# Kernel optimization log

Hardware: AMD Instinct MI355X
Metric: run time of the kernel (lower is better)

Reference implementation:

```python
import jax, jax.numpy as jnp
import numpy as np
from jax import lax

C = 256
HEADS = 8
HD = C // HEADS  # 32
D = 32  # max(L=32, C//16)
KERNELS = [1, 3, 5, 7]
EPS = 1e-5


def setup_inputs() -> dict:
    key = jax.random.key(0)
    ks = jax.random.split(key, 16)
    inp = {
        'x': jax.random.normal(ks[0], (8, C, 32, 32), jnp.float32),
        'qkv_w': jax.random.normal(ks[1], (3 * C, C), jnp.float32) * 0.05,
        'out_w': jax.random.normal(ks[2], (C, C), jnp.float32) * 0.05,
        'conv_w1': jax.random.normal(ks[3], (C, C, 1, 1), jnp.float32) * 0.05,
        'conv_w3': jax.random.normal(ks[4], (C, C, 3, 3), jnp.float32) * 0.05,
        'conv_w5': jax.random.normal(ks[5], (C, C, 5, 5), jnp.float32) * 0.05,
        'conv_w7': jax.random.normal(ks[6], (C, C, 7, 7), jnp.float32) * 0.05,
        'conv_b': jax.random.normal(ks[7], (4, C), jnp.float32) * 0.05,
        'bn_gamma': jax.random.uniform(ks[8], (4, C), jnp.float32, 0.5, 1.5),
        'bn_beta': jax.random.normal(ks[9], (4, C), jnp.float32) * 0.05,
        'bn_mean': jax.random.normal(ks[10], (4, C), jnp.float32) * 0.05,
        'bn_var': jax.random.uniform(ks[11], (4, C), jnp.float32, 0.5, 1.5),
        'fc_w': jax.random.normal(ks[12], (D, C), jnp.float32) * 0.05,
        'fc_b': jax.random.normal(ks[13], (D,), jnp.float32) * 0.05,
        'fcs_w': jax.random.normal(ks[14], (4, C, D), jnp.float32) * 0.05,
        'fcs_b': jax.random.normal(ks[15], (4, C), jnp.float32) * 0.05,
    }
    return inp


def _conv_bn_relu(x, w, b, g, beta, m, v):
    k = w.shape[-1]
    y = lax.conv_general_dilated(
        x, w, window_strides=(1, 1), padding=[(k // 2, k // 2)] * 2,
        dimension_numbers=('NCHW', 'OIHW', 'NCHW'))
    y = y + b[None, :, None, None]
    inv = g / jnp.sqrt(v + EPS)  # eval-mode batchnorm
    y = y * inv[None, :, None, None] + (beta - m * inv)[None, :, None, None]
    return jax.nn.relu(y)


def reference(x, qkv_w, out_w, conv_w1, conv_w3, conv_w5, conv_w7, conv_b,
              bn_gamma, bn_beta, bn_mean, bn_var, fc_w, fc_b, fcs_w, fcs_b):
    bsz, ch, ht, wd = x.shape
    n = ht * wd
    xf = x.reshape(bsz, ch, n)
    qkv = jnp.einsum('oc,bcn->bon', qkv_w, xf)  # [b, 3C, N] (1x1 conv)
    q, k, v = jnp.split(qkv, 3, axis=1)
    q = q.reshape(bsz, HEADS, HD, n)
    k = k.reshape(bsz, HEADS, HD, n)
    v = v.reshape(bsz, HEADS, HD, n)
    scale = 1.0 / np.sqrt(HD)
    scores = jnp.einsum('bhdi,bhdj->bhij', q, k) * scale  # [b,h,N,N]
    probs = jax.nn.softmax(scores, axis=-1)
    ctx = jnp.einsum('bhij,bhdj->bhdi', probs, v)  # [b,h,hd,N]
    ctx = ctx.reshape(bsz, ch, ht, wd)
    out = jnp.einsum('oc,bcn->bon', out_w, ctx.reshape(bsz, ch, n)).reshape(bsz, ch, ht, wd)

    ws = [conv_w1, conv_w3, conv_w5, conv_w7]
    feats = jnp.stack([
        _conv_bn_relu(out, ws[i], conv_b[i], bn_gamma[i], bn_beta[i], bn_mean[i], bn_var[i])
        for i in range(4)
    ], axis=0)  # [4, b, C, H, W]
    U = feats.sum(axis=0)
    S = U.mean(axis=(-2, -1))  # [b, C]
    Z = S @ fc_w.T + fc_b  # [b, D]
    logits = jnp.einsum('kcd,bd->kbc', fcs_w, Z) + fcs_b[:, None, :]  # [4,b,C]
    attn = jax.nn.softmax(logits, axis=0)[:, :, :, None, None]  # softmax over kernel branches
    V = (attn * feats).sum(axis=0)  # [b, C, H, W]
    return V
```

## Files before the change

### kernel.cpp

```cpp
#include <hip/hip_runtime.h>
#include <math.h>


typedef __attribute__((ext_vector_type(8))) short bf16x8;
typedef __attribute__((ext_vector_type(4))) float f32x4;

__device__ __forceinline__ ushort f2bf(float f) {
  uint32_t u = __float_as_uint(f);
  u += 0x7fffu + ((u >> 16) & 1u);
  return (ushort)(u >> 16);
}

__device__ __forceinline__ uint cvt_pk(float lo, float hi) {
  uint r;
  asm volatile("v_cvt_pk_bf16_f32 %0, %1, %2" : "=v"(r) : "v"(lo), "v"(hi));
  return r;
}

__global__ __launch_bounds__(256) void pad_cvt(const float* __restrict__ src,
                                               ushort* __restrict__ dst) {
  __shared__ ushort t[32][258];
  int y = blockIdx.x, b = blockIdx.y, tid = threadIdx.x;
  for (int u = 0; u < 32; ++u) {
    int idx = u * 256 + tid;
    int c = idx >> 5, p = idx & 31;
    t[p][c] = f2bf(src[(((size_t)b * 256 + c) << 10) + (y << 5) + p]);
  }
  __syncthreads();
  for (int u = 0; u < 32; ++u) {
    int idx = u * 256 + tid;
    int p = idx >> 8, c = idx & 255;
    dst[(((size_t)b * 38 + y + 3) * 38 + p + 3) * 256 + c] = t[p][c];
  }
}

template <int KK>
__global__ __launch_bounds__(256) void repack(const float* __restrict__ src,
                                              ushort* __restrict__ dst, int M) {
  __shared__ ushort t[256][KK + 1];
  int co = blockIdx.x, tid = threadIdx.x;
  for (int idx = tid; idx < 256 * KK; idx += 256) {
    int ci = idx / KK, k = idx - ci * KK;
    t[ci][k] = f2bf(src[(size_t)co * 256 * KK + idx]);
  }
  __syncthreads();
  for (int idx = tid; idx < 256 * KK; idx += 256) {
    int k = idx >> 8, ci = idx & 255;
    dst[((size_t)k * M + co) * 256 + ci] = t[ci][k];
  }
}

__global__ void bn_fold(const float* __restrict__ cb, const float* __restrict__ g,
                        const float* __restrict__ be, const float* __restrict__ mn,
                        const float* __restrict__ v, float* __restrict__ binv,
                        float* __restrict__ bb2) {
  int i = threadIdx.x;
  float inv = g[i] * rsqrtf(v[i] + 1e-5f);
  binv[i] = inv;
  bb2[i] = be[i] + (cb[i] - mn[i]) * inv;
}

template <int MODE>
__device__ __forceinline__ void conv_core(
    const ushort* __restrict__ W, const ushort* __restrict__ X,
    float* __restrict__ outF, ushort* __restrict__ outU,
    int M, int KS, int b, int co0, int pxt, int cs0, int cs1, bool accum,
    char* smem) {
  const int R = KS >> 1;
  const int NT = KS * KS;
  const int NR = 4 + 2 * R;
  const int NPIX = NR * 38;
  char* Bs = smem;
  char* As = smem + 24320;
  const int tid = threadIdx.x;
  const int w = tid >> 6, l = tid & 63, lr = l & 15, sg = l >> 4;
  const int y0 = pxt * 4;
  const ushort* Xb = X + ((size_t)b * 38 + (y0 + 3 - R)) * 38 * 256;

  f32x4 acc[4][4] = {};

  auto stageA = [&](int t, int ci0, int bufsel) {
    const ushort* Wt = W + ((size_t)t * M + co0) * 256 + ci0;
    char* dbase = As + (bufsel << 13) + (w << 11);
#pragma unroll
    for (int u = 0; u < 2; ++u) {
      int idx16 = (w * 2 + u) * 64 + l;
      int co = idx16 >> 2, s = idx16 & 3;
      const ushort* src = Wt + (size_t)co * 256 + ((s ^ ((co >> 1) & 3)) << 3);
      __builtin_amdgcn_global_load_lds(
          (const __attribute__((address_space(1))) void*)src,
          (__attribute__((address_space(3))) void*)(dbase + (u << 10)), 16, 0, 0);
    }
  };

  int g = 0;
  stageA(0, cs0 << 5, 0);
  const int u_stg = (NPIX * 4 + 255) >> 8;
  for (int cs = cs0; cs < cs1; ++cs) {
    int ci0 = cs << 5;
    for (int u = 0; u < u_stg; ++u) {
      int idx = (u << 8) + tid;
      if (idx < NPIX * 4) {
        int pix = idx >> 2, s = idx & 3;
        int pr = pix / 38, pc = pix - pr * 38;
        const ushort* srcp = Xb + ((size_t)(pr * 38 + pc)) * 256 + ci0 +
                             ((s ^ ((pc >> 1) & 3)) << 3);
        __builtin_amdgcn_global_load_lds(
            (const __attribute__((address_space(1))) void*)srcp,
            (__attribute__((address_space(3))) void*)(Bs + (u << 12) + (w << 10)),
            16, 0, 0);
      }
    }
    __syncthreads();
    int dy = 0, dx = 0;
    for (int t = 0; t < NT; ++t) {
      if (t + 1 < NT) stageA(t + 1, ci0, (g + 1) & 1);
      else if (cs + 1 < cs1) stageA(0, ci0 + 32, (g + 1) & 1);

      bf16x8 af[4], bfr[4];
      char* Ab = As + ((g & 1) << 13);
#pragma unroll
      for (int fa = 0; fa < 4; ++fa) {
        int co = (w & 1) * 64 + fa * 16 + lr;
        af[fa] = *(const bf16x8*)(Ab + (co << 6) + ((sg ^ ((co >> 1) & 3)) << 4));
      }
      int rowbase = (w >> 1) * 2 + dy;
      int cbase = dx + 3 - R + lr;
#pragma unroll
      for (int fp = 0; fp < 4; ++fp) {
        int lrow = rowbase + (fp >> 1);
        int pc = cbase + ((fp & 1) << 4);
        bfr[fp] = *(const bf16x8*)(Bs + ((lrow * 38 + pc) << 6) +
                                   ((sg ^ ((pc >> 1) & 3)) << 4));
      }
#pragma unroll
      for (int fa = 0; fa < 4; ++fa)
#pragma unroll
        for (int fp = 0; fp < 4; ++fp)
          acc[fa][fp] = __builtin_amdgcn_mfma_f32_16x16x32_bf16(
              af[fa], bfr[fp], acc[fa][fp], 0, 0, 0);
      ++g;
      if (++dx == KS) { dx = 0; ++dy; }
      __syncthreads();
    }
  }
  int coB = co0 + (w & 1) * 64;
  int pxB = pxt * 128 + (w >> 1) * 64;
#pragma unroll
  for (int fa = 0; fa < 4; ++fa) {
#pragma unroll
    for (int fp = 0; fp < 4; ++fp) {
      int px = pxB + (fp >> 1) * 32 + (fp & 1) * 16 + lr;
      int cobase = coB + fa * 16 + 4 * sg;
      f32x4 v4 = acc[fa][fp];
      if (MODE == 2) {
#pragma unroll
        for (int r = 0; r < 4; ++r) {
          int co = cobase + r;
          float* dst = &outF[((size_t)b * M + co) * 1024 + px];
          if (accum) unsafeAtomicAdd(dst, v4[r]);
          else *dst = v4[r];
        }
      } else if (MODE == 1) {
        int y = px >> 5, x = px & 31;
        ushort* dst = outU + ((size_t)(b * 38 + y + 3) * 38 + x + 3) * 256 + cobase;
        *(uint*)dst = cvt_pk(v4[0], v4[1]);
        *(uint*)(dst + 2) = cvt_pk(v4[2], v4[3]);
      } else {
        if (coB < 256) {
          int h = cobase >> 5, d = cobase & 31;
          ushort* dst = outU + ((size_t)(b * 8 + h) * 1024 + px) * 32 + d;
          const float sc = 0.17677669529663687f;
          *(uint*)dst = cvt_pk(v4[0] * sc, v4[1] * sc);
          *(uint*)(dst + 2) = cvt_pk(v4[2] * sc, v4[3] * sc);
        } else if (coB < 512) {
          int c2 = cobase - 256;
          int h = c2 >> 5, d = c2 & 31;
          ushort* dst = outU + 2097152 + ((size_t)(b * 8 + h) * 1024 + px) * 32 + d;
          *(uint*)dst = cvt_pk(v4[0], v4[1]);
          *(uint*)(dst + 2) = cvt_pk(v4[2], v4[3]);
        } else {
          int c2 = cobase - 512;
#pragma unroll
          for (int r = 0; r < 4; ++r)
            outU[4194304 + ((size_t)(b * 256 + c2 + r)) * 1024 + px] = f2bf(v4[r]);
        }
      }
    }
  }
}

__global__ __launch_bounds__(256, 2) void gemm_qkv(const ushort* __restrict__ W,
                                                   const ushort* __restrict__ X,
                                                   ushort* __restrict__ U) {
  __shared__ __align__(16) char smem[40704];
  int cot = blockIdx.x >> 3, pxt = blockIdx.x & 7, b = blockIdx.y;
  conv_core<0>(W, X, nullptr, U, 768, 1, b, cot * 128, pxt, 0, 8, false, smem);
}

__global__ __launch_bounds__(256, 2) void gemm_oproj(const ushort* __restrict__ W,
                                                     const ushort* __restrict__ X,
                                                     ushort* __restrict__ U) {
  __shared__ __align__(16) char smem[40704];
  int cot = blockIdx.x >> 3, pxt = blockIdx.x & 7, b = blockIdx.y;
  conv_core<1>(W, X, nullptr, U, 256, 1, b, cot * 128, pxt, 0, 8, false, smem);
}

__global__ __launch_bounds__(256, 4) void conv_fused(const ushort* __restrict__ Wc,
                                                     const ushort* __restrict__ X,
                                                     float* __restrict__ feats) {
  __shared__ __align__(16) char smem[40704];
  int gx = blockIdx.x;
  int br, cs0, cs1;
  bool accum;
  int sub = gx & 127;
  if (gx < 512) {
    br = 3; int ch = gx >> 7; cs0 = ch * 2; cs1 = cs0 + 2; accum = true;
  } else if (gx < 768) {
    br = 2; int ch = (gx >> 7) & 1; cs0 = ch * 4; cs1 = cs0 + 4; accum = true;
  } else if (gx < 896) {
    br = 1; cs0 = 0; cs1 = 8; accum = false;
  } else {
    br = 0; cs0 = 0; cs1 = 8; accum = false;
  }
  int pxt = sub & 7, cot = (sub >> 3) & 1, b = sub >> 4;
  const int ksarr[4] = {1, 3, 5, 7};
  const int wofs[4] = {0, 65536, 655360, 2293760};
  conv_core<2>(Wc + wofs[br], X, feats + (size_t)br * 2097152, nullptr, 256,
               ksarr[br], b, cot * 128, pxt, cs0, cs1, accum, smem);
}

__global__ __launch_bounds__(256, 2) void flash_attn(const ushort* __restrict__ QKV,
                                                     ushort* __restrict__ P2out) {
  __shared__ __align__(16) char smem[24576];
  const int tid = threadIdx.x, w = tid >> 6, l = tid & 63, lr = l & 15, sg = l >> 4;
  char* Ks = smem;
  char* Vs = smem + 4096;
  char* Ps = smem + 8192 + (w << 12);
  int bh = blockIdx.y, b = bh >> 3, h = bh & 7;
  const ushort* QT = QKV + (size_t)bh * 32768;
  const ushort* KT = QKV + 2097152 + (size_t)bh * 32768;
  const ushort* VT = QKV + 4194304 + (size_t)(b * 256 + h * 32) * 1024;
  int ibase = blockIdx.x * 128 + w * 32;

  bf16x8 qf[2];
#pragma unroll
  for (int i16 = 0; i16 < 2; ++i16)
    qf[i16] = *(const bf16x8*)(QT + ((size_t)(ibase + i16 * 16 + lr)) * 32 + sg * 8);

  f32x4 oacc[4] = {};
  float mrow[2] = {-3e30f, -3e30f};
  float lrow[2] = {0.f, 0.f};

  for (int jb = 0; jb < 1024; jb += 64) {
    {
      int j = tid >> 2, s = tid & 3;
      const ushort* srcK = KT + (size_t)(jb + j) * 32 + ((s ^ ((j >> 1) & 3)) << 3);
      __builtin_amdgcn_global_load_lds(
          (const __attribute__((address_space(1))) void*)srcK,
          (__attribute__((address_space(3))) void*)(Ks + (w << 10)), 16, 0, 0);
      int d = tid >> 3, s2 = tid & 7;
      const ushort* srcV = VT + (size_t)d * 1024 + jb + ((s2 ^ (d & 7)) << 3);
      __builtin_amdgcn_global_load_lds(
          (const __attribute__((address_space(1))) void*)srcV,
          (__attribute__((address_space(3))) void*)(Vs + (w << 10)), 16, 0, 0);
    }
    __syncthreads();

    bf16x8 kf[4];
#pragma unroll
    for (int jt = 0; jt < 4; ++jt) {
      int j = jt * 16 + lr;
      kf[jt] = *(const bf16x8*)(Ks + j * 64 + ((sg ^ ((j >> 1) & 3)) << 4));
    }
    f32x4 sac[2][4] = {};
#pragma unroll
    for (int i16 = 0; i16 < 2; ++i16)
#pragma unroll
      for (int jt = 0; jt < 4; ++jt)
        sac[i16][jt] = __builtin_amdgcn_mfma_f32_16x16x32_bf16(
            kf[jt], qf[i16], sac[i16][jt], 0, 0, 0);

#pragma unroll
    for (int i16 = 0; i16 < 2; ++i16) {
      float tmax = sac[i16][0][0];
#pragma unroll
      for (int jt = 0; jt < 4; ++jt)
#pragma unroll
        for (int r = 0; r < 4; ++r) tmax = fmaxf(tmax, sac[i16][jt][r]);
      tmax = fmaxf(tmax, __shfl_xor(tmax, 16));
      tmax = fmaxf(tmax, __shfl_xor(tmax, 32));
      float mnew = fmaxf(mrow[i16], tmax);
      float fac = __expf(mrow[i16] - mnew);
      mrow[i16] = mnew;
      float psum = 0.f;
      int i = i16 * 16 + lr;
      char* prow = Ps + i * 128;
#pragma unroll
      for (int jt = 0; jt < 4; ++jt) {
        float p0 = __expf(sac[i16][jt][0] - mnew);
        float p1 = __expf(sac[i16][jt][1] - mnew);
        float p2 = __expf(sac[i16][jt][2] - mnew);
        float p3 = __expf(sac[i16][jt][3] - mnew);
        psum += (p0 + p1) + (p2 + p3);
        int j0 = jt * 16 + sg * 4;
        uint* dst = (uint*)(prow + (((j0 >> 3) ^ (i & 7)) << 4) + ((j0 & 7) << 1));
        dst[0] = cvt_pk(p0, p1);
        dst[1] = cvt_pk(p2, p3);
      }
      lrow[i16] = lrow[i16] * fac + psum;
#pragma unroll
      for (int d16 = 0; d16 < 2; ++d16)
#pragma unroll
        for (int r = 0; r < 4; ++r) oacc[d16 * 2 + i16][r] *= fac;
    }
    asm volatile("s_waitcnt lgkmcnt(0)" ::: "memory");

#pragma unroll
    for (int h2 = 0; h2 < 2; ++h2) {
      bf16x8 vf[2], pf[2];
#pragma unroll
      for (int d16 = 0; d16 < 2; ++d16) {
        int d = d16 * 16 + lr;
        vf[d16] = *(const bf16x8*)(Vs + d * 128 + ((((h2 << 2) + sg) ^ (d & 7)) << 4));
      }
#pragma unroll
      for (int i16 = 0; i16 < 2; ++i16) {
        int i = i16 * 16 + lr;
        pf[i16] = *(const bf16x8*)(Ps + i * 128 + ((((h2 << 2) + sg) ^ (i & 7)) << 4));
      }
#pragma unroll
      for (int d16 = 0; d16 < 2; ++d16)
#pragma unroll
        for (int i16 = 0; i16 < 2; ++i16)
          oacc[d16 * 2 + i16] = __builtin_amdgcn_mfma_f32_16x16x32_bf16(
              vf[d16], pf[i16], oacc[d16 * 2 + i16], 0, 0, 0);
    }
    __syncthreads();
  }

  float linv[2];
#pragma unroll
  for (int i16 = 0; i16 < 2; ++i16) {
    float lt = lrow[i16];
    lt += __shfl_xor(lt, 16);
    lt += __shfl_xor(lt, 32);
    linv[i16] = 1.0f / lt;
  }
#pragma unroll
  for (int i16 = 0; i16 < 2; ++i16) {
    int i = ibase + i16 * 16 + lr;
    int y = i >> 5, x = i & 31;
    ushort* dst0 = P2out + ((size_t)(b * 38 + y + 3) * 38 + x + 3) * 256 + h * 32 + sg * 4;
#pragma unroll
    for (int d16 = 0; d16 < 2; ++d16) {
      f32x4 v = oacc[d16 * 2 + i16];
      ushort* dst = dst0 + d16 * 16;
      *(uint*)dst = cvt_pk(v[0] * linv[i16], v[1] * linv[i16]);
      *(uint*)(dst + 2) = cvt_pk(v[2] * linv[i16], v[3] * linv[i16]);
    }
  }
}

__global__ __launch_bounds__(256) void reduce_s(const float* __restrict__ feats,
                                                const float* __restrict__ binv,
                                                const float* __restrict__ bb2,
                                                float* __restrict__ S) {
  int bc = blockIdx.x;
  int c = bc & 255;
  const float* p = feats + (size_t)bc * 1024;
  float s = 0;
#pragma unroll
  for (int k = 0; k < 4; ++k) {
    float bi = binv[k * 256 + c], bo = bb2[k * 256 + c];
#pragma unroll
    for (int u = 0; u < 4; ++u)
      s += fmaxf(fmaf(p[(size_t)k * 2097152 + u * 256 + threadIdx.x], bi, bo), 0.f);
  }
  __shared__ float red[256];
  red[threadIdx.x] = s;
  __syncthreads();
  for (int off = 128; off > 0; off >>= 1) {
    if (threadIdx.x < off) red[threadIdx.x] += red[threadIdx.x + off];
    __syncthreads();
  }
  if (threadIdx.x == 0) S[bc] = red[0] * (1.0f / 1024.0f);
}

__global__ __launch_bounds__(256) void fc_attn_k(
    const float* __restrict__ S, const float* __restrict__ fc_w,
    const float* __restrict__ fc_b, const float* __restrict__ fcs_w,
    const float* __restrict__ fcs_b, float* __restrict__ attnw) {
  int b = blockIdx.x;
  __shared__ float Ss[256];
  __shared__ float Zs[32];
  int tid = threadIdx.x;
  Ss[tid] = S[b * 256 + tid];
  __syncthreads();
  if (tid < 32) {
    float z = fc_b[tid];
    for (int c = 0; c < 256; ++c) z += Ss[c] * fc_w[tid * 256 + c];
    Zs[tid] = z;
  }
  __syncthreads();
  int c = tid;
  float lg[4];
#pragma unroll
  for (int k = 0; k < 4; ++k) {
    float v = fcs_b[k * 256 + c];
    const float* wp = &fcs_w[((size_t)k * 256 + c) * 32];
#pragma unroll
    for (int d = 0; d < 32; ++d) v += wp[d] * Zs[d];
    lg[k] = v;
  }
  float m = fmaxf(fmaxf(lg[0], lg[1]), fmaxf(lg[2], lg[3]));
  float e0 = __expf(lg[0] - m), e1 = __expf(lg[1] - m);
  float e2 = __expf(lg[2] - m), e3 = __expf(lg[3] - m);
  float inv = 1.0f / (e0 + e1 + e2 + e3);
  attnw[(0 * 8 + b) * 256 + c] = e0 * inv;
  attnw[(1 * 8 + b) * 256 + c] = e1 * inv;
  attnw[(2 * 8 + b) * 256 + c] = e2 * inv;
  attnw[(3 * 8 + b) * 256 + c] = e3 * inv;
}

__global__ __launch_bounds__(256) void combine_k(const float* __restrict__ feats,
                                                 const float* __restrict__ attnw,
                                                 const float* __restrict__ binv,
                                                 const float* __restrict__ bb2,
                                                 float* __restrict__ out) {
  size_t idx = (size_t)blockIdx.x * 256 + threadIdx.x;
  int c = (int)((idx >> 10) & 255);
  int b = (int)(idx >> 18);
  float s = 0;
#pragma unroll
  for (int k = 0; k < 4; ++k) {
    float v = fmaxf(fmaf(feats[(size_t)k * 2097152 + idx],
                         binv[k * 256 + c], bb2[k * 256 + c]), 0.f);
    s += attnw[(k * 8 + b) * 256 + c] * v;
  }
  out[idx] = s;
}

extern "C" void kernel_launch(void* const* d_in, const int* in_sizes, int n_in,
                              void* d_out, int out_size, void* d_ws, size_t ws_size,
                              hipStream_t stream) {
  (void)in_sizes; (void)n_in; (void)out_size; (void)ws_size;
  const float* x      = (const float*)d_in[0];
  const float* qkv_w  = (const float*)d_in[1];
  const float* out_w  = (const float*)d_in[2];
  const float* cw1    = (const float*)d_in[3];
  const float* cw3    = (const float*)d_in[4];
  const float* cw5    = (const float*)d_in[5];
  const float* cw7    = (const float*)d_in[6];
  const float* conv_b = (const float*)d_in[7];
  const float* bn_g   = (const float*)d_in[8];
  const float* bn_b   = (const float*)d_in[9];
  const float* bn_m   = (const float*)d_in[10];
  const float* bn_v   = (const float*)d_in[11];
  const float* fc_w   = (const float*)d_in[12];
  const float* fc_b   = (const float*)d_in[13];
  const float* fcs_w  = (const float*)d_in[14];
  const float* fcs_b  = (const float*)d_in[15];

  char*  wsb   = (char*)d_ws;
  float* wsf   = (float*)d_ws;
  ushort* QKVb = (ushort*)d_ws;
  float* feats = wsf;
  float* S     = wsf + 10485760;
  float* attnw = wsf + 10487808;
  ushort* P1   = (ushort*)(wsb + 41984000);
  ushort* P2   = (ushort*)(wsb + 47898624);
  ushort* Wq   = (ushort*)(wsb + 53813248);
  ushort* Wo   = (ushort*)(wsb + 54206464);
  ushort* Wc   = (ushort*)(wsb + 54337536);
  float* binv  = (float*)(wsb + 65347584);
  float* bb2   = (float*)(wsb + 65351680);
  float* out   = (float*)d_out;

  hipMemsetAsync(P1, 0, 2 * 5914624, stream);
  hipMemsetAsync(wsb + 16777216, 0, 16777216, stream);
  bn_fold<<<1, 1024, 0, stream>>>(conv_b, bn_g, bn_b, bn_m, bn_v, binv, bb2);
  repack<1><<<768, 256, 0, stream>>>(qkv_w, Wq, 768);
  repack<1><<<256, 256, 0, stream>>>(out_w, Wo, 256);
  repack<1><<<256, 256, 0, stream>>>(cw1, Wc, 256);
  repack<9><<<256, 256, 0, stream>>>(cw3, Wc + 65536, 256);
  repack<25><<<256, 256, 0, stream>>>(cw5, Wc + 655360, 256);
  repack<49><<<256, 256, 0, stream>>>(cw7, Wc + 2293760, 256);

  pad_cvt<<<dim3(32, 8), 256, 0, stream>>>(x, P1);
  gemm_qkv<<<dim3(48, 8), 256, 0, stream>>>(Wq, P1, QKVb);
  flash_attn<<<dim3(8, 64), 256, 0, stream>>>(QKVb, P2);
  gemm_oproj<<<dim3(16, 8), 256, 0, stream>>>(Wo, P2, P1);
  conv_fused<<<dim3(1024), 256, 0, stream>>>(Wc, P1, feats);

  reduce_s<<<2048, 256, 0, stream>>>(feats, binv, bb2, S);
  fc_attn_k<<<8, 256, 0, stream>>>(S, fc_w, fc_b, fcs_w, fcs_b, attnw);
  combine_k<<<8192, 256, 0, stream>>>(feats, attnw, binv, bb2, out);
}
```

Measured before the change: 232.9 us.

## Merge prep kernels, relax conv barriers, set MFMA priority, rebalance conv branches

Eight small preprocessing launches (bn_fold, six weight repacks, input pad/convert) become one prep_all kernel that dispatches on block index, cutting launch overhead. In the conv inner loop, __syncthreads is replaced by explicit s_waitcnt vmcnt(2)/s_barrier so the just-issued prefetch can stay in flight, and s_setprio raises wave priority around the MFMA block. The 3x3 branch is split over channel halves with atomic accumulation, and the 1x1 conv is folded into some of those blocks, which needs an extra memset of the 3x3 output buffer. The hand-written waitcnt assumes a fixed number of outstanding loads per stage, which risks reading data that has not landed if that count is wrong, and the extra atomics and memset add traffic.

```diff
diff --git a/kernel.cpp b/kernel.cpp
--- a/kernel.cpp
+++ b/kernel.cpp
@@ -17,10 +17,29 @@
   return r;
 }
 
-__global__ __launch_bounds__(256) void pad_cvt(const float* __restrict__ src,
-                                               ushort* __restrict__ dst) {
-  __shared__ ushort t[32][258];
-  int y = blockIdx.x, b = blockIdx.y, tid = threadIdx.x;
+
+template <int KK>
+__device__ __forceinline__ void repack_dev(const float* __restrict__ src,
+                                           ushort* __restrict__ dst, int M, int co,
+                                           char* smraw) {
+  ushort(*t)[KK + 1] = (ushort(*)[KK + 1])smraw;
+  int tid = threadIdx.x;
+  for (int idx = tid; idx < 256 * KK; idx += 256) {
+    int ci = idx / KK, k = idx - ci * KK;
+    t[ci][k] = f2bf(src[(size_t)co * 256 * KK + idx]);
+  }
+  __syncthreads();
+  for (int idx = tid; idx < 256 * KK; idx += 256) {
+    int k = idx >> 8, ci = idx & 255;
+    dst[((size_t)k * M + co) * 256 + ci] = t[ci][k];
+  }
+}
+
+__device__ __forceinline__ void pad_dev(const float* __restrict__ src,
+                                        ushort* __restrict__ dst, int y, int b,
+                                        char* smraw) {
+  ushort(*t)[258] = (ushort(*)[258])smraw;
+  int tid = threadIdx.x;
   for (int u = 0; u < 32; ++u) {
     int idx = u * 256 + tid;
     int c = idx >> 5, p = idx & 31;
@@ -34,30 +53,34 @@
   }
 }
 
-template <int KK>
-__global__ __launch_bounds__(256) void repack(const float* __restrict__ src,
-                                              ushort* __restrict__ dst, int M) {
-  __shared__ ushort t[256][KK + 1];
-  int co = blockIdx.x, tid = threadIdx.x;
-  for (int idx = tid; idx < 256 * KK; idx += 256) {
-    int ci = idx / KK, k = idx - ci * KK;
-    t[ci][k] = f2bf(src[(size_t)co * 256 * KK + idx]);
-  }
-  __syncthreads();
-  for (int idx = tid; idx < 256 * KK; idx += 256) {
-    int k = idx >> 8, ci = idx & 255;
-    dst[((size_t)k * M + co) * 256 + ci] = t[ci][k];
-  }
-}
-
-__global__ void bn_fold(const float* __restrict__ cb, const float* __restrict__ g,
-                        const float* __restrict__ be, const float* __restrict__ mn,
-                        const float* __restrict__ v, float* __restrict__ binv,
-                        float* __restrict__ bb2) {
-  int i = threadIdx.x;
-  float inv = g[i] * rsqrtf(v[i] + 1e-5f);
-  binv[i] = inv;
-  bb2[i] = be[i] + (cb[i] - mn[i]) * inv;
+__global__ __launch_bounds__(256) void prep_all(
+    const float* __restrict__ qkv_w, const float* __restrict__ out_w,
+    const float* __restrict__ cw1, const float* __restrict__ cw3,
+    const float* __restrict__ cw5, const float* __restrict__ cw7,
+    ushort* __restrict__ Wq, ushort* __restrict__ Wo, ushort* __restrict__ Wc,
+    const float* __restrict__ x, ushort* __restrict__ P1,
+    const float* __restrict__ cb, const float* __restrict__ g,
+    const float* __restrict__ be, const float* __restrict__ mn,
+    const float* __restrict__ v, float* __restrict__ binv, float* __restrict__ bb2) {
+  __shared__ __align__(16) char sm[25600];
+  int gx = blockIdx.x;
+  if (gx < 768) repack_dev<1>(qkv_w, Wq, 768, gx, sm);
+  else if (gx < 1024) repack_dev<1>(out_w, Wo, 256, gx - 768, sm);
+  else if (gx < 1280) repack_dev<1>(cw1, Wc, 256, gx - 1024, sm);
+  else if (gx < 1536) repack_dev<9>(cw3, Wc + 65536, 256, gx - 1280, sm);
+  else if (gx < 1792) repack_dev<25>(cw5, Wc + 655360, 256, gx - 1536, sm);
+  else if (gx < 2048) repack_dev<49>(cw7, Wc + 2293760, 256, gx - 1792, sm);
+  else if (gx < 2304) pad_dev(x, P1, (gx - 2048) & 31, (gx - 2048) >> 5, sm);
+  else {
+    int tid = threadIdx.x;
+#pragma unroll
+    for (int u = 0; u < 4; ++u) {
+      int i = u * 256 + tid;
+      float inv = g[i] * rsqrtf(v[i] + 1e-5f);
+      binv[i] = inv;
+      bb2[i] = be[i] + (cb[i] - mn[i]) * inv;
+    }
+  }
 }
 
 template <int MODE>
@@ -114,8 +137,14 @@
     __syncthreads();
     int dy = 0, dx = 0;
     for (int t = 0; t < NT; ++t) {
+      bool staged = true;
       if (t + 1 < NT) stageA(t + 1, ci0, (g + 1) & 1);
       else if (cs + 1 < cs1) stageA(0, ci0 + 32, (g + 1) & 1);
+      else staged = false;
+      if (staged)
+        asm volatile("s_waitcnt vmcnt(2)\n\ts_barrier" ::: "memory");
+      else
+        asm volatile("s_waitcnt vmcnt(0)\n\ts_barrier" ::: "memory");
 
       bf16x8 af[4], bfr[4];
       char* Ab = As + ((g & 1) << 13);
@@ -133,15 +162,17 @@
         bfr[fp] = *(const bf16x8*)(Bs + ((lrow * 38 + pc) << 6) +
                                    ((sg ^ ((pc >> 1) & 3)) << 4));
       }
+      __builtin_amdgcn_s_setprio(1);
 #pragma unroll
       for (int fa = 0; fa < 4; ++fa)
 #pragma unroll
         for (int fp = 0; fp < 4; ++fp)
           acc[fa][fp] = __builtin_amdgcn_mfma_f32_16x16x32_bf16(
               af[fa], bfr[fp], acc[fa][fp], 0, 0, 0);
+      __builtin_amdgcn_s_setprio(0);
       ++g;
       if (++dx == KS) { dx = 0; ++dy; }
-      __syncthreads();
+      asm volatile("s_barrier" ::: "memory");
     }
   }
   int coB = co0 + (w & 1) * 64;
@@ -211,23 +242,25 @@
                                                      float* __restrict__ feats) {
   __shared__ __align__(16) char smem[40704];
   int gx = blockIdx.x;
+  int sub = gx & 127;
+  int pxt = sub & 7, cot = (sub >> 3) & 1, b = sub >> 4;
   int br, cs0, cs1;
-  bool accum;
-  int sub = gx & 127;
   if (gx < 512) {
-    br = 3; int ch = gx >> 7; cs0 = ch * 2; cs1 = cs0 + 2; accum = true;
+    br = 3; int ch = gx >> 7; cs0 = ch * 2; cs1 = cs0 + 2;
   } else if (gx < 768) {
-    br = 2; int ch = (gx >> 7) & 1; cs0 = ch * 4; cs1 = cs0 + 4; accum = true;
-  } else if (gx < 896) {
-    br = 1; cs0 = 0; cs1 = 8; accum = false;
+    br = 2; int ch = (gx >> 7) & 1; cs0 = ch * 4; cs1 = cs0 + 4;
   } else {
-    br = 0; cs0 = 0; cs1 = 8; accum = false;
-  }
-  int pxt = sub & 7, cot = (sub >> 3) & 1, b = sub >> 4;
+    br = 1; int ch = (gx >> 7) & 1; cs0 = ch * 4; cs1 = cs0 + 4;
+  }
   const int ksarr[4] = {1, 3, 5, 7};
   const int wofs[4] = {0, 65536, 655360, 2293760};
   conv_core<2>(Wc + wofs[br], X, feats + (size_t)br * 2097152, nullptr, 256,
-               ksarr[br], b, cot * 128, pxt, cs0, cs1, accum, smem);
+               ksarr[br], b, cot * 128, pxt, cs0, cs1, true, smem);
+  if (gx >= 768 && gx < 896) {
+    __syncthreads();
+    conv_core<2>(Wc, X, feats, nullptr, 256, 1, b, cot * 128, pxt, 0, 8, false,
+                 smem);
+  }
 }
 
 __global__ __launch_bounds__(256, 2) void flash_attn(const ushort* __restrict__ QKV,
@@ -479,17 +512,13 @@
 
   hipMemsetAsync(P1, 0, 2 * 5914624, stream);
   hipMemsetAsync(wsb + 16777216, 0, 16777216, stream);
-  bn_fold<<<1, 1024, 0, stream>>>(conv_b, bn_g, bn_b, bn_m, bn_v, binv, bb2);
-  repack<1><<<768, 256, 0, stream>>>(qkv_w, Wq, 768);
-  repack<1><<<256, 256, 0, stream>>>(out_w, Wo, 256);
-  repack<1><<<256, 256, 0, stream>>>(cw1, Wc, 256);
-  repack<9><<<256, 256, 0, stream>>>(cw3, Wc + 65536, 256);
-  repack<25><<<256, 256, 0, stream>>>(cw5, Wc + 655360, 256);
-  repack<49><<<256, 256, 0, stream>>>(cw7, Wc + 2293760, 256);
-
-  pad_cvt<<<dim3(32, 8), 256, 0, stream>>>(x, P1);
+  prep_all<<<2305, 256, 0, stream>>>(qkv_w, out_w, cw1, cw3, cw5, cw7, Wq, Wo, Wc,
+                                     x, P1, conv_b, bn_g, bn_b, bn_m, bn_v, binv,
+                                     bb2);
+
   gemm_qkv<<<dim3(48, 8), 256, 0, stream>>>(Wq, P1, QKVb);
   flash_attn<<<dim3(8, 64), 256, 0, stream>>>(QKVb, P2);
+  hipMemsetAsync(wsb + 8388608, 0, 8388608, stream);
   gemm_oproj<<<dim3(16, 8), 256, 0, stream>>>(Wo, P2, P1);
   conv_fused<<<dim3(1024), 256, 0, stream>>>(Wc, P1, feats);
 
```

Measured after the change: 221.3 us. 5.0% less time.
